# Kernel tuning notes

Hardware: AMD Instinct MI355X
Metric: run time of the kernel (lower is better)

The kernel has to match this reference:

```python
import jax, jax.numpy as jnp
import numpy as np

B, L, D = 4, 2048, 2048
H = 16
DH = D // H           # 128
DC = 512              # d_kv_compress


def rotate_half(x):
    x1, x2 = jnp.split(x, 2, axis=-1)
    return jnp.concatenate([-x2, x1], axis=-1)


def apply_rotary_emb(x, cos, sin):
    return x * cos + rotate_half(x) * sin


def setup_inputs() -> dict:
    key = jax.random.key(0)
    ks = jax.random.split(key, 8)
    s = 1.0 / np.sqrt(D)
    sc = 1.0 / np.sqrt(DC)
    return {
        "x": jax.random.normal(ks[0], (B, L, D), jnp.float32),
        "rope_cos": jax.random.uniform(ks[1], (B, L, DH), jnp.float32),
        "rope_sin": jax.random.uniform(ks[2], (B, L, DH), jnp.float32),
        # weights stored as (out, in) like nn.Linear
        "W_q": jax.random.normal(ks[3], (D, D), jnp.float32) * s,
        "W_dkv": jax.random.normal(ks[4], (DC, D), jnp.float32) * s,
        "W_uk": jax.random.normal(ks[5], (D, DC), jnp.float32) * sc,
        "W_uv": jax.random.normal(ks[6], (D, DC), jnp.float32) * sc,
        "W_o": jax.random.normal(ks[7], (D, D), jnp.float32) * s,
    }


def reference(x, rope_cos, rope_sin, W_q, W_dkv, W_uk, W_uv, W_o):
    scale = DH ** (-0.5)
    # projections: y = x @ W.T
    Q = (x @ W_q.T).reshape(B, L, H, DH).transpose(0, 2, 1, 3)    # [B,H,L,DH]
    c_kv = x @ W_dkv.T                                            # [B,L,DC]
    K = (c_kv @ W_uk.T).reshape(B, L, H, DH).transpose(0, 2, 1, 3)
    V = (c_kv @ W_uv.T).reshape(B, L, H, DH).transpose(0, 2, 1, 3)
    cos = rope_cos[:, None, :, :]  # [B,1,L,DH]
    sin = rope_sin[:, None, :, :]
    Q = apply_rotary_emb(Q, cos, sin)
    K = apply_rotary_emb(K, cos, sin)
    # non-causal SDPA
    scores = jnp.einsum("bhqd,bhkd->bhqk", Q, K) * scale
    attn = jax.nn.softmax(scores, axis=-1)
    out = jnp.einsum("bhqk,bhkd->bhqd", attn, V)                  # [B,H,L,DH]
    out = out.transpose(0, 2, 1, 3).reshape(B, L, D)
    return out @ W_o.T
```

## Files before the change

### kernel.cpp

```cpp
#include <hip/hip_runtime.h>
#include <math.h>

typedef __attribute__((ext_vector_type(8))) short bf16x8;
typedef __attribute__((ext_vector_type(4))) float f32x4;
typedef __attribute__((ext_vector_type(16))) float f32x16;

#define NB 4
#define NL 2048
#define ND 2048
#define NH 16
#define NDH 128
#define NDC 512
#define NROWS (NB*NL)

__device__ __forceinline__ unsigned short f2bf(float f) {
  unsigned int u = __float_as_uint(f);
  u += 0x7fffu + ((u >> 16) & 1u);
  return (unsigned short)(u >> 16);
}
__device__ __forceinline__ float bf2f(unsigned short h) {
  return __uint_as_float(((unsigned int)h) << 16);
}
__device__ __forceinline__ unsigned int cvtpk(float lo, float hi) {
  unsigned int r;
  asm("v_cvt_pk_bf16_f32 %0, %1, %2" : "=v"(r) : "v"(lo), "v"(hi));
  return r;
}
__device__ __forceinline__ void permswap(unsigned int &a, unsigned int &b) {
  asm("v_permlane32_swap_b32 %0, %1" : "+v"(a), "+v"(b));
}
__device__ __forceinline__ float exp2_fast(float x) {
  float r; asm("v_exp_f32 %0, %1" : "=v"(r) : "v"(x)); return r;
}

__device__ __forceinline__ void gld16(const void* g, void* l) {
  __builtin_amdgcn_global_load_lds((const __attribute__((address_space(1))) void*)g,
                                   (__attribute__((address_space(3))) void*)l, 16, 0, 0);
}

__global__ void cvt_kernel(const float4* __restrict__ in, ushort4* __restrict__ out, int n4) {
  int stride = gridDim.x * blockDim.x;
  for (int i = blockIdx.x * blockDim.x + threadIdx.x; i < n4; i += stride) {
    float4 v = in[i];
    ushort4 o;
    o.x = f2bf(v.x); o.y = f2bf(v.y); o.z = f2bf(v.z); o.w = f2bf(v.w);
    out[i] = o;
  }
}

template<int OUT_F32>
__global__ __launch_bounds__(256) void gemm_nt(const unsigned short* __restrict__ A,
                                               const unsigned short* __restrict__ Bm,
                                               void* __restrict__ Cv,
                                               int M, int N, int K) {
  __shared__ unsigned short As[128 * 32];
  __shared__ unsigned short Bs[128 * 32];
  const int tid = threadIdx.x;
  const int wid = tid >> 6;
  const int lane = tid & 63;
  const int wr = wid >> 1, wc = wid & 1;
  const long bm = blockIdx.y, bn = blockIdx.x;
  const int r15 = lane & 15;
  const int koff = (lane >> 4) * 8;
  const int srow = lane >> 2;
  const int scol = (lane & 3) * 8;

  f32x4 acc[4][4];
#pragma unroll
  for (int m = 0; m < 4; ++m)
#pragma unroll
    for (int n = 0; n < 4; ++n) acc[m][n] = (f32x4){0.f, 0.f, 0.f, 0.f};

  const unsigned short* Ablk = A + (bm * 128 + wid * 16 + srow) * (long)K + scol;
  const unsigned short* Bblk = Bm + (bn * 128 + wid * 16 + srow) * (long)K + scol;
  unsigned short* AsW = As + wid * 16 * 32;
  unsigned short* BsW = Bs + wid * 16 * 32;

  for (int kk = 0; kk < K; kk += 32) {
    __syncthreads();
#pragma unroll
    for (int j = 0; j < 2; ++j) {
      gld16(Ablk + (long)j * 64 * K + kk, AsW + j * 64 * 32);
      gld16(Bblk + (long)j * 64 * K + kk, BsW + j * 64 * 32);
    }
    __syncthreads();
    bf16x8 af[4], bfr[4];
#pragma unroll
    for (int m = 0; m < 4; ++m)
      af[m] = *(const bf16x8*)(As + (wr * 64 + m * 16 + r15) * 32 + koff);
#pragma unroll
    for (int n = 0; n < 4; ++n)
      bfr[n] = *(const bf16x8*)(Bs + (wc * 64 + n * 16 + r15) * 32 + koff);
#pragma unroll
    for (int m = 0; m < 4; ++m)
#pragma unroll
      for (int n = 0; n < 4; ++n)
        acc[m][n] = __builtin_amdgcn_mfma_f32_16x16x32_bf16(af[m], bfr[n], acc[m][n], 0, 0, 0);
  }

  const int rr = (lane >> 4) * 4;
#pragma unroll
  for (int m = 0; m < 4; ++m) {
#pragma unroll
    for (int n = 0; n < 4; ++n) {
      long row0 = bm * 128 + wr * 64 + m * 16 + rr;
      long col = bn * 128 + wc * 64 + n * 16 + r15;
#pragma unroll
      for (int r = 0; r < 4; ++r) {
        float v = acc[m][n][r];
        if (OUT_F32) ((float*)Cv)[(row0 + r) * (long)N + col] = v;
        else ((unsigned short*)Cv)[(row0 + r) * (long)N + col] = f2bf(v);
      }
    }
  }
}

template<int OUT_F32>
__global__ __launch_bounds__(512) void gemm_nt256(const unsigned short* __restrict__ A,
                                                  const unsigned short* __restrict__ Bm,
                                                  void* __restrict__ Cv,
                                                  int M, int N, int K) {
  __shared__ unsigned short lds[2][2][16384];
  const int tid = threadIdx.x;
  const int wid = tid >> 6, lane = tid & 63;
  const int wm = wid >> 2, wn = wid & 3;
  const int r15 = lane & 15, khi = lane >> 4;

  const int gx = gridDim.x;
  int bid = blockIdx.y * gx + blockIdx.x;
  int cpx = (gx * gridDim.y) >> 3;
  int swz = (bid & 7) * cpx + (bid >> 3);
  const long bm = swz / gx, bn = swz % gx;

  const int c0 = tid, c1 = 512 + tid;
  const int r0 = c0 >> 3, r1 = c1 >> 3;
  const int cs0 = ((c0 & 7) ^ (r0 & 7)) * 8;
  const int cs1 = ((c1 & 7) ^ (r1 & 7)) * 8;
  const unsigned short* srcA = A + (bm * 256) * (long)K;
  const unsigned short* srcB = Bm + (bn * 256) * (long)K;

#define STAGE256(mat, h, kb, bufi) do {                                              \
    const unsigned short* s_ = (mat) ? srcB : srcA;                                  \
    gld16(s_ + ((h) * 128 + r0) * (long)K + (kb) + cs0,                              \
          &lds[bufi][mat][(h) * 8192 + wid * 512]);                                  \
    gld16(s_ + ((h) * 128 + r1) * (long)K + (kb) + cs1,                              \
          &lds[bufi][mat][(h) * 8192 + 4096 + wid * 512]);                           \
  } while (0)

  f32x4 acc[8][4];
#pragma unroll
  for (int m = 0; m < 8; ++m)
#pragma unroll
    for (int n = 0; n < 4; ++n) acc[m][n] = (f32x4){0.f, 0.f, 0.f, 0.f};

  const int NT = K >> 6;
  STAGE256(0, 0, 0, 0); STAGE256(0, 1, 0, 0);
  STAGE256(1, 0, 0, 0); STAGE256(1, 1, 0, 0);

  for (int t = 0; t < NT; ++t) {
    const int buf = t & 1, nbuf = buf ^ 1;
    const int kb1 = (t + 1) << 6;
    const bool pf = (t + 1 < NT);
    __builtin_amdgcn_s_barrier();
    if (pf) {
      STAGE256(0, 0, kb1, nbuf);
      asm volatile("s_waitcnt vmcnt(2)" ::: "memory");
    } else {
      asm volatile("s_waitcnt vmcnt(0)" ::: "memory");
    }
    __builtin_amdgcn_s_barrier();

    bf16x8 bfr[4][2];
#pragma unroll
    for (int n = 0; n < 4; ++n)
#pragma unroll
      for (int kk = 0; kk < 2; ++kk) {
        int rb = wn * 64 + n * 16 + r15;
        bfr[n][kk] = *(const bf16x8*)&lds[buf][1][rb * 64 + (((kk * 4 + khi) ^ (rb & 7)) * 8)];
      }
#pragma unroll
    for (int mb = 0; mb < 4; ++mb) {
      if (mb != 0) {
        __builtin_amdgcn_s_barrier();
        if (pf) {
          if (mb == 1) STAGE256(0, 1, kb1, nbuf);
          else if (mb == 2) STAGE256(1, 0, kb1, nbuf);
          else STAGE256(1, 1, kb1, nbuf);
        }
      }
      bf16x8 af[2][2];
#pragma unroll
      for (int m2 = 0; m2 < 2; ++m2)
#pragma unroll
        for (int kk = 0; kk < 2; ++kk) {
          int ra = wm * 128 + mb * 32 + m2 * 16 + r15;
          af[m2][kk] = *(const bf16x8*)&lds[buf][0][ra * 64 + (((kk * 4 + khi) ^ (ra & 7)) * 8)];
        }
      asm volatile("s_waitcnt lgkmcnt(0)" ::: "memory");
      __builtin_amdgcn_sched_barrier(0);
      __builtin_amdgcn_s_setprio(1);
#pragma unroll
      for (int m2 = 0; m2 < 2; ++m2)
#pragma unroll
        for (int n = 0; n < 4; ++n)
#pragma unroll
          for (int kk = 0; kk < 2; ++kk)
            acc[mb * 2 + m2][n] = __builtin_amdgcn_mfma_f32_16x16x32_bf16(
                af[m2][kk], bfr[n][kk], acc[mb * 2 + m2][n], 0, 0, 0);
      __builtin_amdgcn_s_setprio(0);
    }
  }
#undef STAGE256

#pragma unroll
  for (int mi = 0; mi < 8; ++mi) {
#pragma unroll
    for (int n = 0; n < 4; ++n) {
      long row0 = bm * 256 + wm * 128 + mi * 16 + khi * 4;
      long col = bn * 256 + wn * 64 + n * 16 + r15;
#pragma unroll
      for (int r = 0; r < 4; ++r) {
        float v = acc[mi][n][r];
        if (OUT_F32) ((float*)Cv)[(row0 + r) * (long)N + col] = v;
        else ((unsigned short*)Cv)[(row0 + r) * (long)N + col] = f2bf(v);
      }
    }
  }
}

__global__ void rope_kernel(unsigned short* __restrict__ Qb, const float* __restrict__ cosb,
                            const float* __restrict__ sinb, float scale) {
  const long row = blockIdx.x;
  const float* cr = cosb + row * NDH;
  const float* sr = sinb + row * NDH;
  unsigned short* q = Qb + row * (long)ND;
  for (int p = threadIdx.x; p < NH * 64; p += blockDim.x) {
    int h = p >> 6, d = p & 63;
    int i1 = h * 128 + d, i2 = i1 + 64;
    float q1 = bf2f(q[i1]), q2 = bf2f(q[i2]);
    float c1 = cr[d], c2 = cr[d + 64], s1 = sr[d], s2 = sr[d + 64];
    float o1 = (q1 * c1 - q2 * s1) * scale;
    float o2 = (q2 * c2 + q1 * s2) * scale;
    q[i1] = f2bf(o1);
    q[i2] = f2bf(o2);
  }
}

__global__ __launch_bounds__(512) void flash_attn(const unsigned short* __restrict__ Qb,
                                                  const unsigned short* __restrict__ Kb,
                                                  const unsigned short* __restrict__ Vb,
                                                  unsigned short* __restrict__ Ob) {
  __shared__ unsigned short KsArr[2 * 8192];
  __shared__ unsigned int VtArr[2 * 4608];

  const int tid = threadIdx.x, wid = tid >> 6, lane = tid & 63;
  const int l31 = lane & 31, hi5 = lane >> 5;

  const int L = blockIdx.y * 8 + blockIdx.x;
  const int bh = ((L >> 6) << 3) | (L & 7);
  const int qt = (L >> 3) & 7;
  const int b = bh >> 4, h = bh & 15;
  const long rowbase = (long)b * NL;
  const int colbase = h * NDH;
  const long q0 = (long)qt * 256 + wid * 32;

  bf16x8 qf[8];
  {
    const unsigned short* qp = Qb + (rowbase + q0 + l31) * (long)ND + colbase + hi5 * 8;
#pragma unroll
    for (int kc = 0; kc < 8; ++kc) qf[kc] = *(const bf16x8*)(qp + kc * 16);
  }

  f32x16 oacc[4];
#pragma unroll
  for (int db = 0; db < 4; ++db)
#pragma unroll
    for (int i = 0; i < 16; ++i) oacc[db][i] = 0.f;
  float mrun = -1e30f, lrun = 0.f;

  const int kp = tid >> 4;
  const int c8 = (tid & 15) * 8;
  bf16x8 kreg[2], vreg[2];

#define LOAD_KV(kt_) do {                                                          \
    _Pragma("unroll") for (int j = 0; j < 2; ++j) {                                \
      const long grow = (rowbase + (kt_) * 64 + 2 * kp + j) * (long)ND + colbase + c8; \
      kreg[j] = *(const bf16x8*)(Kb + grow);                                       \
      vreg[j] = *(const bf16x8*)(Vb + grow);                                       \
    } } while (0)

#define WRITE_KV(bi) do {                                                          \
    _Pragma("unroll") for (int j = 0; j < 2; ++j) {                                \
      int row_ = 2 * kp + j;                                                       \
      *(bf16x8*)(KsArr + (bi) * 8192 + row_ * 128 + (c8 ^ ((row_ & 15) << 3))) = kreg[j]; \
    }                                                                              \
    _Pragma("unroll") for (int i = 0; i < 8; ++i) {                                \
      int d_ = c8 + i;                                                             \
      VtArr[(bi) * 4608 + d_ * 36 + 4 * ((kp >> 2) ^ ((d_ >> 3) & 7)) + (kp & 3)] = \
          (unsigned int)(unsigned short)vreg[0][i] |                               \
          ((unsigned int)(unsigned short)vreg[1][i] << 16);                        \
    } } while (0)

  LOAD_KV(0);
  WRITE_KV(0);
  __syncthreads();
  LOAD_KV(1);

  const int NT = NL / 64;
  for (int kt = 0; kt < NT; ++kt) {
    const int bf = kt & 1;
    const unsigned short* Ksb = KsArr + bf * 8192;
    const unsigned int* Vtb = VtArr + bf * 4608;

    f32x16 sacc[2];
    __builtin_amdgcn_s_setprio(1);
#pragma unroll
    for (int nb = 0; nb < 2; ++nb) {
#pragma unroll
      for (int i = 0; i < 16; ++i) sacc[nb][i] = 0.f;
#pragma unroll
      for (int kc = 0; kc < 8; ++kc) {
        int row = nb * 32 + l31;
        bf16x8 kf = *(const bf16x8*)(Ksb + row * 128 + ((kc * 16 + hi5 * 8) ^ ((row & 15) << 3)));
        sacc[nb] = __builtin_amdgcn_mfma_f32_32x32x16_bf16(kf, qf[kc], sacc[nb], 0, 0, 0);
      }
    }
    __builtin_amdgcn_s_setprio(0);

    if (kt + 1 < NT) WRITE_KV(bf ^ 1);
    if (kt + 2 < NT) LOAD_KV(kt + 2);

    float mxa[8];
#pragma unroll
    for (int i = 0; i < 8; ++i)
      mxa[i] = fmaxf(fmaxf(sacc[0][i], sacc[0][i + 8]), fmaxf(sacc[1][i], sacc[1][i + 8]));
    float mx = fmaxf(fmaxf(fmaxf(mxa[0], mxa[1]), fmaxf(mxa[2], mxa[3])),
                     fmaxf(fmaxf(mxa[4], mxa[5]), fmaxf(mxa[6], mxa[7])));
    mx = fmaxf(mx, __shfl_xor(mx, 32));
    if (!__all(mx - mrun <= 8.f)) {
      float mnew = fmaxf(mrun, mx);
      float corr = exp2_fast(mrun - mnew);
      mrun = mnew;
      lrun *= corr;
#pragma unroll
      for (int db = 0; db < 4; ++db)
#pragma unroll
        for (int i = 0; i < 16; ++i) oacc[db][i] *= corr;
    }
    float s4[4] = {0.f, 0.f, 0.f, 0.f};
#pragma unroll
    for (int nb = 0; nb < 2; ++nb)
#pragma unroll
      for (int r = 0; r < 16; ++r) {
        float e = exp2_fast(sacc[nb][r] - mrun);
        sacc[nb][r] = e;
        s4[r & 3] += e;
      }
    float s = (s4[0] + s4[1]) + (s4[2] + s4[3]);
    s += __shfl_xor(s, 32);
    lrun += s;

    union { unsigned int u[4]; bf16x8 v; } pa[2][2];
#pragma unroll
    for (int nb = 0; nb < 2; ++nb) {
      unsigned int x1 = cvtpk(sacc[nb][0], sacc[nb][1]);
      unsigned int x2 = cvtpk(sacc[nb][2], sacc[nb][3]);
      unsigned int y1 = cvtpk(sacc[nb][4], sacc[nb][5]);
      unsigned int y2 = cvtpk(sacc[nb][6], sacc[nb][7]);
      unsigned int z1 = cvtpk(sacc[nb][8], sacc[nb][9]);
      unsigned int z2 = cvtpk(sacc[nb][10], sacc[nb][11]);
      unsigned int w1 = cvtpk(sacc[nb][12], sacc[nb][13]);
      unsigned int w2 = cvtpk(sacc[nb][14], sacc[nb][15]);
      permswap(x1, y1);
      permswap(x2, y2);
      permswap(z1, w1);
      permswap(z2, w2);
      pa[nb][0].u[0] = x1; pa[nb][0].u[1] = x2; pa[nb][0].u[2] = y1; pa[nb][0].u[3] = y2;
      pa[nb][1].u[0] = z1; pa[nb][1].u[1] = z2; pa[nb][1].u[2] = w1; pa[nb][1].u[3] = w2;
    }

    __builtin_amdgcn_s_setprio(1);
#pragma unroll
    for (int db = 0; db < 4; ++db) {
      int d = db * 32 + l31;
      int dsw = (d >> 3) & 7;
#pragma unroll
      for (int nb = 0; nb < 2; ++nb)
#pragma unroll
        for (int ks = 0; ks < 2; ++ks) {
          int g = nb * 4 + ks * 2 + hi5;
          bf16x8 vf = *(const bf16x8*)(Vtb + d * 36 + 4 * (g ^ dsw));
          oacc[db] = __builtin_amdgcn_mfma_f32_32x32x16_bf16(vf, pa[nb][ks].v, oacc[db], 0, 0, 0);
        }
    }
    __builtin_amdgcn_s_setprio(0);
    __syncthreads();
  }
#undef LOAD_KV
#undef WRITE_KV

  float rinv = 1.0f / lrun;
  unsigned short* scr = (unsigned short*)VtArr + wid * 2304;
#pragma unroll
  for (int c = 0; c < 2; ++c) {
    asm volatile("s_waitcnt lgkmcnt(0)" ::: "memory");
    __builtin_amdgcn_sched_barrier(0);
#pragma unroll
    for (int dbh = 0; dbh < 2; ++dbh) {
      int db = 2 * c + dbh;
#pragma unroll
      for (int t = 0; t < 8; ++t) {
        int d_lo = dbh * 32 + ((2 * t) & 3) + 8 * (t >> 1) + 4 * hi5;
        unsigned int pv = cvtpk(oacc[db][2 * t] * rinv, oacc[db][2 * t + 1] * rinv);
        *(unsigned int*)(scr + l31 * 72 + d_lo) = pv;
      }
    }
    asm volatile("s_waitcnt lgkmcnt(0)" ::: "memory");
    __builtin_amdgcn_sched_barrier(0);
#pragma unroll
    for (int j = 0; j < 4; ++j) {
      int row = j * 8 + (lane >> 3);
      bf16x8 ov = *(const bf16x8*)(scr + row * 72 + (lane & 7) * 8);
      *(bf16x8*)(Ob + (rowbase + q0 + row) * (long)ND + colbase + c * 64 + (lane & 7) * 8) = ov;
    }
  }
}

extern "C" void kernel_launch(void* const* d_in, const int* in_sizes, int n_in,
                              void* d_out, int out_size, void* d_ws, size_t ws_size,
                              hipStream_t stream) {
  const float* x = (const float*)d_in[0];
  const float* rope_cos = (const float*)d_in[1];
  const float* rope_sin = (const float*)d_in[2];
  const float* W_q = (const float*)d_in[3];
  const float* W_dkv = (const float*)d_in[4];
  const float* W_uk = (const float*)d_in[5];
  const float* W_uv = (const float*)d_in[6];
  const float* W_o = (const float*)d_in[7];
  float* out = (float*)d_out;

  char* p = (char*)d_ws;
  unsigned short* xb = (unsigned short*)p;    p += (size_t)NROWS * ND * 2;
  unsigned short* Wqb = (unsigned short*)p;   p += (size_t)ND * ND * 2;
  unsigned short* Wdkvb = (unsigned short*)p; p += (size_t)NDC * ND * 2;
  unsigned short* Wukb = (unsigned short*)p;  p += (size_t)ND * NDC * 2;
  unsigned short* Wuvb = (unsigned short*)p;  p += (size_t)ND * NDC * 2;
  unsigned short* Wob = (unsigned short*)p;   p += (size_t)ND * ND * 2;
  unsigned short* Qb = (unsigned short*)p;    p += (size_t)NROWS * ND * 2;
  unsigned short* ckv = (unsigned short*)p;   p += (size_t)NROWS * NDC * 2;
  unsigned short* Kbf = (unsigned short*)p;   p += (size_t)NROWS * ND * 2;
  unsigned short* Vbf = (unsigned short*)p;   p += (size_t)NROWS * ND * 2;
  unsigned short* AO = (unsigned short*)p;    p += (size_t)NROWS * ND * 2;

  {
    struct { const float* s; unsigned short* d; long n; } cv[6] = {
      {x, xb, (long)NROWS * ND},
      {W_q, Wqb, (long)ND * ND},
      {W_dkv, Wdkvb, (long)NDC * ND},
      {W_uk, Wukb, (long)ND * NDC},
      {W_uv, Wuvb, (long)ND * NDC},
      {W_o, Wob, (long)ND * ND},
    };
    for (int i = 0; i < 6; ++i) {
      int n4 = (int)(cv[i].n / 4);
      int blocks = (n4 + 255) / 256;
      if (blocks > 2048) blocks = 2048;
      cvt_kernel<<<blocks, 256, 0, stream>>>((const float4*)cv[i].s, (ushort4*)cv[i].d, n4);
    }
  }

  gemm_nt256<0><<<dim3(ND / 256, NROWS / 256), 512, 0, stream>>>(xb, Wqb, Qb, NROWS, ND, ND);
  gemm_nt<0><<<dim3(NDC / 128, NROWS / 128), 256, 0, stream>>>(xb, Wdkvb, ckv, NROWS, NDC, ND);
  gemm_nt256<0><<<dim3(ND / 256, NROWS / 256), 512, 0, stream>>>(ckv, Wukb, Kbf, NROWS, ND, NDC);
  gemm_nt256<0><<<dim3(ND / 256, NROWS / 256), 512, 0, stream>>>(ckv, Wuvb, Vbf, NROWS, ND, NDC);

  const float scale_q = 0.08838834764831845f * 1.4426950408889634f;
  rope_kernel<<<NROWS, 256, 0, stream>>>(Qb, rope_cos, rope_sin, scale_q);
  rope_kernel<<<NROWS, 256, 0, stream>>>(Kbf, rope_cos, rope_sin, 1.0f);

  flash_attn<<<dim3(8, NB * NH * 8 / 8), 512, 0, stream>>>(Qb, Kbf, Vbf, AO);

  gemm_nt256<1><<<dim3(ND / 256, NROWS / 256), 512, 0, stream>>>(AO, Wob, out, NROWS, ND, ND);
}
```

Measured before the change: 447.6 us.

## Process two query sub-tiles per wave in flash attention and vectorize rope

Each wave in flash attention now handles 64 query rows as two 32-row sets, so every K/V fragment read from LDS feeds two MFMAs. The block covers 512 queries and the grid halves to 256 blocks. The aim is to halve K/V global and LDS traffic per query and amortize loads and barriers. The cost is roughly double the accumulator and Q registers, so occupancy drops, and with only 256 blocks the CUs may be underfilled. The rope kernel is also rewritten to use 8-wide vector loads and stores with 128 threads per row.

```diff
diff --git a/kernel.cpp b/kernel.cpp
--- a/kernel.cpp
+++ b/kernel.cpp
@@ -231,19 +231,32 @@
 __global__ void rope_kernel(unsigned short* __restrict__ Qb, const float* __restrict__ cosb,
                             const float* __restrict__ sinb, float scale) {
   const long row = blockIdx.x;
+  const int p = threadIdx.x;
+  const int h = p >> 3, d8 = (p & 7) * 8;
   const float* cr = cosb + row * NDH;
   const float* sr = sinb + row * NDH;
-  unsigned short* q = Qb + row * (long)ND;
-  for (int p = threadIdx.x; p < NH * 64; p += blockDim.x) {
-    int h = p >> 6, d = p & 63;
-    int i1 = h * 128 + d, i2 = i1 + 64;
-    float q1 = bf2f(q[i1]), q2 = bf2f(q[i2]);
-    float c1 = cr[d], c2 = cr[d + 64], s1 = sr[d], s2 = sr[d + 64];
-    float o1 = (q1 * c1 - q2 * s1) * scale;
-    float o2 = (q2 * c2 + q1 * s2) * scale;
-    q[i1] = f2bf(o1);
-    q[i2] = f2bf(o2);
-  }
+  unsigned short* q = Qb + row * (long)ND + h * 128 + d8;
+
+  bf16x8 qlo = *(const bf16x8*)(q);
+  bf16x8 qhi = *(const bf16x8*)(q + 64);
+  float4 c0 = *(const float4*)(cr + d8), c1 = *(const float4*)(cr + d8 + 4);
+  float4 c2 = *(const float4*)(cr + d8 + 64), c3 = *(const float4*)(cr + d8 + 68);
+  float4 s0 = *(const float4*)(sr + d8), s1 = *(const float4*)(sr + d8 + 4);
+  float4 s2 = *(const float4*)(sr + d8 + 64), s3 = *(const float4*)(sr + d8 + 68);
+  float cl[8] = {c0.x, c0.y, c0.z, c0.w, c1.x, c1.y, c1.z, c1.w};
+  float ch[8] = {c2.x, c2.y, c2.z, c2.w, c3.x, c3.y, c3.z, c3.w};
+  float sl[8] = {s0.x, s0.y, s0.z, s0.w, s1.x, s1.y, s1.z, s1.w};
+  float sh[8] = {s2.x, s2.y, s2.z, s2.w, s3.x, s3.y, s3.z, s3.w};
+  bf16x8 olo, ohi;
+#pragma unroll
+  for (int i = 0; i < 8; ++i) {
+    float q1 = bf2f((unsigned short)qlo[i]);
+    float q2 = bf2f((unsigned short)qhi[i]);
+    olo[i] = (short)f2bf((q1 * cl[i] - q2 * sl[i]) * scale);
+    ohi[i] = (short)f2bf((q2 * ch[i] + q1 * sh[i]) * scale);
+  }
+  *(bf16x8*)(q) = olo;
+  *(bf16x8*)(q + 64) = ohi;
 }
 
 __global__ __launch_bounds__(512) void flash_attn(const unsigned short* __restrict__ Qb,
@@ -257,26 +270,31 @@
   const int l31 = lane & 31, hi5 = lane >> 5;
 
   const int L = blockIdx.y * 8 + blockIdx.x;
-  const int bh = ((L >> 6) << 3) | (L & 7);
-  const int qt = (L >> 3) & 7;
+  const int bh = ((L >> 5) << 3) | (L & 7);
+  const int qt = (L >> 3) & 3;
   const int b = bh >> 4, h = bh & 15;
   const long rowbase = (long)b * NL;
   const int colbase = h * NDH;
-  const long q0 = (long)qt * 256 + wid * 32;
-
-  bf16x8 qf[8];
+  const long q0 = (long)qt * 512 + wid * 64;
+
+  bf16x8 qfA[8], qfB[8];
   {
-    const unsigned short* qp = Qb + (rowbase + q0 + l31) * (long)ND + colbase + hi5 * 8;
-#pragma unroll
-    for (int kc = 0; kc < 8; ++kc) qf[kc] = *(const bf16x8*)(qp + kc * 16);
-  }
-
-  f32x16 oacc[4];
+    const unsigned short* qpA = Qb + (rowbase + q0 + l31) * (long)ND + colbase + hi5 * 8;
+    const unsigned short* qpB = qpA + 32 * (long)ND;
+#pragma unroll
+    for (int kc = 0; kc < 8; ++kc) {
+      qfA[kc] = *(const bf16x8*)(qpA + kc * 16);
+      qfB[kc] = *(const bf16x8*)(qpB + kc * 16);
+    }
+  }
+
+  f32x16 oaccA[4], oaccB[4];
 #pragma unroll
   for (int db = 0; db < 4; ++db)
 #pragma unroll
-    for (int i = 0; i < 16; ++i) oacc[db][i] = 0.f;
-  float mrun = -1e30f, lrun = 0.f;
+    for (int i = 0; i < 16; ++i) { oaccA[db][i] = 0.f; oaccB[db][i] = 0.f; }
+  float mrunA = -1e30f, lrunA = 0.f;
+  float mrunB = -1e30f, lrunB = 0.f;
 
   const int kp = tid >> 4;
   const int c8 = (tid & 15) * 8;
@@ -301,6 +319,49 @@
           ((unsigned int)(unsigned short)vreg[1][i] << 16);                        \
     } } while (0)
 
+#define SOFTMAX_PACK(sacc, oacc, mrun, lrun, pa) do {                              \
+    float mxa[8];                                                                  \
+    _Pragma("unroll") for (int i = 0; i < 8; ++i)                                  \
+      mxa[i] = fmaxf(fmaxf(sacc[0][i], sacc[0][i + 8]),                            \
+                     fmaxf(sacc[1][i], sacc[1][i + 8]));                           \
+    float mx = fmaxf(fmaxf(fmaxf(mxa[0], mxa[1]), fmaxf(mxa[2], mxa[3])),          \
+                     fmaxf(fmaxf(mxa[4], mxa[5]), fmaxf(mxa[6], mxa[7])));         \
+    mx = fmaxf(mx, __shfl_xor(mx, 32));                                            \
+    if (!__all(mx - mrun <= 8.f)) {                                                \
+      float mnew = fmaxf(mrun, mx);                                                \
+      float corr = exp2_fast(mrun - mnew);                                         \
+      mrun = mnew;                                                                 \
+      lrun *= corr;                                                                \
+      _Pragma("unroll") for (int db = 0; db < 4; ++db)                             \
+        _Pragma("unroll") for (int i = 0; i < 16; ++i) oacc[db][i] *= corr;        \
+    }                                                                              \
+    float s4[4] = {0.f, 0.f, 0.f, 0.f};                                            \
+    _Pragma("unroll") for (int nb = 0; nb < 2; ++nb)                               \
+      _Pragma("unroll") for (int r = 0; r < 16; ++r) {                             \
+        float e = exp2_fast(sacc[nb][r] - mrun);                                   \
+        sacc[nb][r] = e;                                                           \
+        s4[r & 3] += e;                                                            \
+      }                                                                            \
+    float s = (s4[0] + s4[1]) + (s4[2] + s4[3]);                                   \
+    s += __shfl_xor(s, 32);                                                        \
+    lrun += s;                                                                     \
+    _Pragma("unroll") for (int nb = 0; nb < 2; ++nb) {                             \
+      unsigned int x1 = cvtpk(sacc[nb][0], sacc[nb][1]);                           \
+      unsigned int x2 = cvtpk(sacc[nb][2], sacc[nb][3]);                           \
+      unsigned int y1 = cvtpk(sacc[nb][4], sacc[nb][5]);                           \
+      unsigned int y2 = cvtpk(sacc[nb][6], sacc[nb][7]);                           \
+      unsigned int z1 = cvtpk(sacc[nb][8], sacc[nb][9]);                           \
+      unsigned int z2 = cvtpk(sacc[nb][10], sacc[nb][11]);                         \
+      unsigned int w1 = cvtpk(sacc[nb][12], sacc[nb][13]);                         \
+      unsigned int w2 = cvtpk(sacc[nb][14], sacc[nb][15]);                         \
+      permswap(x1, y1);                                                            \
+      permswap(x2, y2);                                                            \
+      permswap(z1, w1);                                                            \
+      permswap(z2, w2);                                                            \
+      pa[nb][0].u[0] = x1; pa[nb][0].u[1] = x2; pa[nb][0].u[2] = y1; pa[nb][0].u[3] = y2; \
+      pa[nb][1].u[0] = z1; pa[nb][1].u[1] = z2; pa[nb][1].u[2] = w1; pa[nb][1].u[3] = w2; \
+    } } while (0)
+
   LOAD_KV(0);
   WRITE_KV(0);
   __syncthreads();
@@ -312,17 +373,18 @@
     const unsigned short* Ksb = KsArr + bf * 8192;
     const unsigned int* Vtb = VtArr + bf * 4608;
 
-    f32x16 sacc[2];
+    f32x16 saccA[2], saccB[2];
     __builtin_amdgcn_s_setprio(1);
 #pragma unroll
     for (int nb = 0; nb < 2; ++nb) {
 #pragma unroll
-      for (int i = 0; i < 16; ++i) sacc[nb][i] = 0.f;
+      for (int i = 0; i < 16; ++i) { saccA[nb][i] = 0.f; saccB[nb][i] = 0.f; }
 #pragma unroll
       for (int kc = 0; kc < 8; ++kc) {
         int row = nb * 32 + l31;
         bf16x8 kf = *(const bf16x8*)(Ksb + row * 128 + ((kc * 16 + hi5 * 8) ^ ((row & 15) << 3)));
-        sacc[nb] = __builtin_amdgcn_mfma_f32_32x32x16_bf16(kf, qf[kc], sacc[nb], 0, 0, 0);
+        saccA[nb] = __builtin_amdgcn_mfma_f32_32x32x16_bf16(kf, qfA[kc], saccA[nb], 0, 0, 0);
+        saccB[nb] = __builtin_amdgcn_mfma_f32_32x32x16_bf16(kf, qfB[kc], saccB[nb], 0, 0, 0);
       }
     }
     __builtin_amdgcn_s_setprio(0);
@@ -330,54 +392,9 @@
     if (kt + 1 < NT) WRITE_KV(bf ^ 1);
     if (kt + 2 < NT) LOAD_KV(kt + 2);
 
-    float mxa[8];
-#pragma unroll
-    for (int i = 0; i < 8; ++i)
-      mxa[i] = fmaxf(fmaxf(sacc[0][i], sacc[0][i + 8]), fmaxf(sacc[1][i], sacc[1][i + 8]));
-    float mx = fmaxf(fmaxf(fmaxf(mxa[0], mxa[1]), fmaxf(mxa[2], mxa[3])),
-                     fmaxf(fmaxf(mxa[4], mxa[5]), fmaxf(mxa[6], mxa[7])));
-    mx = fmaxf(mx, __shfl_xor(mx, 32));
-    if (!__all(mx - mrun <= 8.f)) {
-      float mnew = fmaxf(mrun, mx);
-      float corr = exp2_fast(mrun - mnew);
-      mrun = mnew;
-      lrun *= corr;
-#pragma unroll
-      for (int db = 0; db < 4; ++db)
-#pragma unroll
-        for (int i = 0; i < 16; ++i) oacc[db][i] *= corr;
-    }
-    float s4[4] = {0.f, 0.f, 0.f, 0.f};
-#pragma unroll
-    for (int nb = 0; nb < 2; ++nb)
-#pragma unroll
-      for (int r = 0; r < 16; ++r) {
-        float e = exp2_fast(sacc[nb][r] - mrun);
-        sacc[nb][r] = e;
-        s4[r & 3] += e;
-      }
-    float s = (s4[0] + s4[1]) + (s4[2] + s4[3]);
-    s += __shfl_xor(s, 32);
-    lrun += s;
-
-    union { unsigned int u[4]; bf16x8 v; } pa[2][2];
-#pragma unroll
-    for (int nb = 0; nb < 2; ++nb) {
-      unsigned int x1 = cvtpk(sacc[nb][0], sacc[nb][1]);
-      unsigned int x2 = cvtpk(sacc[nb][2], sacc[nb][3]);
-      unsigned int y1 = cvtpk(sacc[nb][4], sacc[nb][5]);
-      unsigned int y2 = cvtpk(sacc[nb][6], sacc[nb][7]);
-      unsigned int z1 = cvtpk(sacc[nb][8], sacc[nb][9]);
-      unsigned int z2 = cvtpk(sacc[nb][10], sacc[nb][11]);
-      unsigned int w1 = cvtpk(sacc[nb][12], sacc[nb][13]);
-      unsigned int w2 = cvtpk(sacc[nb][14], sacc[nb][15]);
-      permswap(x1, y1);
-      permswap(x2, y2);
-      permswap(z1, w1);
-      permswap(z2, w2);
-      pa[nb][0].u[0] = x1; pa[nb][0].u[1] = x2; pa[nb][0].u[2] = y1; pa[nb][0].u[3] = y2;
-      pa[nb][1].u[0] = z1; pa[nb][1].u[1] = z2; pa[nb][1].u[2] = w1; pa[nb][1].u[3] = w2;
-    }
+    union { unsigned int u[4]; bf16x8 v; } paA[2][2], paB[2][2];
+    SOFTMAX_PACK(saccA, oaccA, mrunA, lrunA, paA);
+    SOFTMAX_PACK(saccB, oaccB, mrunB, lrunB, paB);
 
     __builtin_amdgcn_s_setprio(1);
 #pragma unroll
@@ -390,7 +407,8 @@
         for (int ks = 0; ks < 2; ++ks) {
           int g = nb * 4 + ks * 2 + hi5;
           bf16x8 vf = *(const bf16x8*)(Vtb + d * 36 + 4 * (g ^ dsw));
-          oacc[db] = __builtin_amdgcn_mfma_f32_32x32x16_bf16(vf, pa[nb][ks].v, oacc[db], 0, 0, 0);
+          oaccA[db] = __builtin_amdgcn_mfma_f32_32x32x16_bf16(vf, paA[nb][ks].v, oaccA[db], 0, 0, 0);
+          oaccB[db] = __builtin_amdgcn_mfma_f32_32x32x16_bf16(vf, paB[nb][ks].v, oaccB[db], 0, 0, 0);
         }
     }
     __builtin_amdgcn_s_setprio(0);
@@ -398,30 +416,36 @@
   }
 #undef LOAD_KV
 #undef WRITE_KV
-
-  float rinv = 1.0f / lrun;
+#undef SOFTMAX_PACK
+
   unsigned short* scr = (unsigned short*)VtArr + wid * 2304;
 #pragma unroll
-  for (int c = 0; c < 2; ++c) {
-    asm volatile("s_waitcnt lgkmcnt(0)" ::: "memory");
-    __builtin_amdgcn_sched_barrier(0);
-#pragma unroll
-    for (int dbh = 0; dbh < 2; ++dbh) {
-      int db = 2 * c + dbh;
-#pragma unroll
-      for (int t = 0; t < 8; ++t) {
-        int d_lo = dbh * 32 + ((2 * t) & 3) + 8 * (t >> 1) + 4 * hi5;
-        unsigned int pv = cvtpk(oacc[db][2 * t] * rinv, oacc[db][2 * t + 1] * rinv);
-        *(unsigned int*)(scr + l31 * 72 + d_lo) = pv;
-      }
-    }
-    asm volatile("s_waitcnt lgkmcnt(0)" ::: "memory");
-    __builtin_amdgcn_sched_barrier(0);
-#pragma unroll
-    for (int j = 0; j < 4; ++j) {
-      int row = j * 8 + (lane >> 3);
-      bf16x8 ov = *(const bf16x8*)(scr + row * 72 + (lane & 7) * 8);
-      *(bf16x8*)(Ob + (rowbase + q0 + row) * (long)ND + colbase + c * 64 + (lane & 7) * 8) = ov;
+  for (int set = 0; set < 2; ++set) {
+    const f32x16* oacc = set ? oaccB : oaccA;
+    float rinv = 1.0f / (set ? lrunB : lrunA);
+    long qset = q0 + set * 32;
+#pragma unroll
+    for (int c = 0; c < 2; ++c) {
+      asm volatile("s_waitcnt lgkmcnt(0)" ::: "memory");
+      __builtin_amdgcn_sched_barrier(0);
+#pragma unroll
+      for (int dbh = 0; dbh < 2; ++dbh) {
+        int db = 2 * c + dbh;
+#pragma unroll
+        for (int t = 0; t < 8; ++t) {
+          int d_lo = dbh * 32 + ((2 * t) & 3) + 8 * (t >> 1) + 4 * hi5;
+          unsigned int pv = cvtpk(oacc[db][2 * t] * rinv, oacc[db][2 * t + 1] * rinv);
+          *(unsigned int*)(scr + l31 * 72 + d_lo) = pv;
+        }
+      }
+      asm volatile("s_waitcnt lgkmcnt(0)" ::: "memory");
+      __builtin_amdgcn_sched_barrier(0);
+#pragma unroll
+      for (int j = 0; j < 4; ++j) {
+        int row = j * 8 + (lane >> 3);
+        bf16x8 ov = *(const bf16x8*)(scr + row * 72 + (lane & 7) * 8);
+        *(bf16x8*)(Ob + (rowbase + qset + row) * (long)ND + colbase + c * 64 + (lane & 7) * 8) = ov;
+      }
     }
   }
 }
@@ -475,10 +499,10 @@
   gemm_nt256<0><<<dim3(ND / 256, NROWS / 256), 512, 0, stream>>>(ckv, Wuvb, Vbf, NROWS, ND, NDC);
 
   const float scale_q = 0.08838834764831845f * 1.4426950408889634f;
-  rope_kernel<<<NROWS, 256, 0, stream>>>(Qb, rope_cos, rope_sin, scale_q);
-  rope_kernel<<<NROWS, 256, 0, stream>>>(Kbf, rope_cos, rope_sin, 1.0f);
-
-  flash_attn<<<dim3(8, NB * NH * 8 / 8), 512, 0, stream>>>(Qb, Kbf, Vbf, AO);
+  rope_kernel<<<NROWS, 128, 0, stream>>>(Qb, rope_cos, rope_sin, scale_q);
+  rope_kernel<<<NROWS, 128, 0, stream>>>(Kbf, rope_cos, rope_sin, 1.0f);
+
+  flash_attn<<<dim3(8, 32), 512, 0, stream>>>(Qb, Kbf, Vbf, AO);
 
   gemm_nt256<1><<<dim3(ND / 256, NROWS / 256), 512, 0, stream>>>(AO, Wob, out, NROWS, ND, ND);
 }
```

After: 702.3 us. 56.9% more time.
